# Kernel tuning notes

Measured on AMD Instinct MI355X. Metric: run time of the kernel, lower is better.

## Reference

```python
import jax, jax.numpy as jnp
import numpy as np

N = 100000
E = 1600000
D = 64  # in = hidden = out channels


def setup_inputs() -> dict:
    key = jax.random.key(0)
    ks = jax.random.split(key, 6)
    x = jax.random.normal(ks[0], (N, D), dtype=jnp.float32)
    edge_index = jax.random.randint(ks[1], (2, E), 0, N, dtype=jnp.int64)
    # bias-free linear weights, torch Linear layout [out, in]
    s = 1.0 / np.sqrt(D)
    W0 = jax.random.uniform(ks[2], (D, D), jnp.float32, -s, s)
    W1 = jax.random.uniform(ks[3], (D, D), jnp.float32, -s, s)
    Wm = jax.random.uniform(ks[4], (D, D), jnp.float32, -s, s)
    eps0 = jnp.zeros((), jnp.float32)  # train_eps=True, init 0.0
    eps1 = jnp.zeros((), jnp.float32)
    return {"x": x, "edge_index": edge_index, "W0": W0, "eps0": eps0,
            "W1": W1, "eps1": eps1, "Wm": Wm}


def reference(x, edge_index, W0, eps0, W1, eps1, Wm):
    n = x.shape[0]
    src, dst = edge_index[0], edge_index[1]

    def gin_conv(h, W, eps):
        # sparse adjacency sum-aggregation: out[i] = sum_{j->i} h[j]
        agg = jax.ops.segment_sum(h[src], dst, num_segments=n)
        # eps-scaled self-loop + bias-free linear
        return (agg + (1.0 + eps) * h) @ W.T

    h1 = jax.nn.relu(gin_conv(x, W0, eps0))   # xs[0], [N, D]
    h2 = jax.nn.relu(gin_conv(h1, W1, eps1))  # xs[1], [N, D]
    return (h1 @ Wm.T + h2) / 2.0
```

## Files before the change

kernel.cpp:

```cpp
#include <hip/hip_runtime.h>


__global__ __launch_bounds__(256) void zero_int_kernel(int* __restrict__ p, int n)
{
    int i = blockIdx.x * blockDim.x + threadIdx.x;
    int stride = gridDim.x * blockDim.x;
    for (; i < n; i += stride) p[i] = 0;
}

__global__ __launch_bounds__(256) void hist_rank_kernel(
    const int* __restrict__ dst, int* __restrict__ deg,
    int* __restrict__ rank, int E)
{
    int base = (blockIdx.x * blockDim.x + threadIdx.x) * 8;
    if (base + 7 < E) {
        int4 a = *(const int4*)&dst[base];
        int4 b = *(const int4*)&dst[base + 4];
        int r0 = atomicAdd(&deg[a.x], 1);
        int r1 = atomicAdd(&deg[a.y], 1);
        int r2 = atomicAdd(&deg[a.z], 1);
        int r3 = atomicAdd(&deg[a.w], 1);
        int r4 = atomicAdd(&deg[b.x], 1);
        int r5 = atomicAdd(&deg[b.y], 1);
        int r6 = atomicAdd(&deg[b.z], 1);
        int r7 = atomicAdd(&deg[b.w], 1);
        *(int4*)&rank[base]     = make_int4(r0, r1, r2, r3);
        *(int4*)&rank[base + 4] = make_int4(r4, r5, r6, r7);
    } else {
        for (int e = base; e < E; ++e) rank[e] = atomicAdd(&deg[dst[e]], 1);
    }
}

__global__ __launch_bounds__(256) void hist_kernel(
    const int* __restrict__ dst, int* __restrict__ deg, int E)
{
    int e4 = (blockIdx.x * blockDim.x + threadIdx.x) * 4;
    if (e4 + 3 < E) {
        int4 d = *(const int4*)&dst[e4];
        atomicAdd(&deg[d.x], 1);
        atomicAdd(&deg[d.y], 1);
        atomicAdd(&deg[d.z], 1);
        atomicAdd(&deg[d.w], 1);
    } else {
        for (int e = e4; e < E; ++e) atomicAdd(&deg[dst[e]], 1);
    }
}

__global__ __launch_bounds__(256) void scanA_kernel(
    const int* __restrict__ deg, int* __restrict__ off,
    int* __restrict__ bsum, int n)
{
    __shared__ int tmp[256];
    int t = threadIdx.x;
    int base = blockIdx.x * 1024 + t * 4;
    int v0 = 0, v1 = 0, v2 = 0, v3 = 0;
    if (base + 3 < n) {
        int4 q = *(const int4*)&deg[base];
        v0 = q.x; v1 = q.y; v2 = q.z; v3 = q.w;
    } else {
        if (base + 0 < n) v0 = deg[base + 0];
        if (base + 1 < n) v1 = deg[base + 1];
        if (base + 2 < n) v2 = deg[base + 2];
    }
    int tot = v0 + v1 + v2 + v3;
    tmp[t] = tot;
    __syncthreads();
    for (int d = 1; d < 256; d <<= 1) {
        int x = (t >= d) ? tmp[t - d] : 0;
        __syncthreads();
        tmp[t] += x;
        __syncthreads();
    }
    int incl = tmp[t];
    int p = incl - tot;
    if (base + 0 < n) off[base + 0] = p;
    if (base + 1 < n) off[base + 1] = p + v0;
    if (base + 2 < n) off[base + 2] = p + v0 + v1;
    if (base + 3 < n) off[base + 3] = p + v0 + v1 + v2;
    if (t == 255) bsum[blockIdx.x] = incl;
}

__global__ __launch_bounds__(256) void scanB_kernel(int* __restrict__ bsum, int nb)
{
    __shared__ int tmp[256];
    int t = threadIdx.x;
    int v = (t < nb) ? bsum[t] : 0;
    tmp[t] = v;
    __syncthreads();
    for (int d = 1; d < 256; d <<= 1) {
        int x = (t >= d) ? tmp[t - d] : 0;
        __syncthreads();
        tmp[t] += x;
        __syncthreads();
    }
    if (t < nb) bsum[t] = tmp[t] - v;
}

__global__ __launch_bounds__(256) void scanC_kernel(
    int* __restrict__ off, int* __restrict__ cursor,
    const int* __restrict__ bsum, int n, int E)
{
    int t = threadIdx.x;
    int add = bsum[blockIdx.x];
    int base = blockIdx.x * 1024 + t * 4;
#pragma unroll
    for (int q = 0; q < 4; ++q) {
        int idx = base + q;
        if (idx < n) {
            int v = off[idx] + add;
            off[idx] = v;
            if (cursor) cursor[idx] = v;
        }
    }
    if (blockIdx.x == 0 && t == 0) off[n] = E;
}

__global__ __launch_bounds__(256) void fill_rank_kernel(
    const int* __restrict__ src, const int* __restrict__ dst,
    const int* __restrict__ rank, const int* __restrict__ off,
    int* __restrict__ bucket, int E)
{
    int base = (blockIdx.x * blockDim.x + threadIdx.x) * 4;
    if (base + 3 < E) {
        int4 d = *(const int4*)&dst[base];
        int4 r = *(const int4*)&rank[base];
        int4 s = *(const int4*)&src[base];
        bucket[off[d.x] + r.x] = s.x;
        bucket[off[d.y] + r.y] = s.y;
        bucket[off[d.z] + r.z] = s.z;
        bucket[off[d.w] + r.w] = s.w;
    } else {
        for (int e = base; e < E; ++e) bucket[off[dst[e]] + rank[e]] = src[e];
    }
}

__global__ __launch_bounds__(256) void fill_kernel(
    const int* __restrict__ src, const int* __restrict__ dst,
    int* __restrict__ cursor, int* __restrict__ bucket, int E)
{
    int e = blockIdx.x * blockDim.x + threadIdx.x;
    if (e < E) {
        int d = dst[e];
        int p = atomicAdd(&cursor[d], 1);
        bucket[p] = src[e];
    }
}

#define WPB 8

__global__ __launch_bounds__(512) void fused_gin_kernel(
    const float* __restrict__ h, const int* __restrict__ off,
    const int* __restrict__ bucket, const float* __restrict__ W,
    const float* __restrict__ eps, float* __restrict__ out, int n)
{
    __shared__ float Ws[64][68];
    __shared__ float P[WPB][4][64];
    __shared__ float rowbuf[WPB][64];
    int tid = threadIdx.x;
    for (int idx = tid; idx < 4096; idx += 512) Ws[idx >> 6][idx & 63] = W[idx];
    __syncthreads();
    float s = 1.0f + eps[0];
    int lane = tid & 63;
    int w = tid >> 6;
    int l16 = lane & 15;
    int g = lane >> 4;
    int wavesTotal = gridDim.x * WPB;
    for (int i = blockIdx.x * WPB + w; i < n; i += wavesTotal) {
        float4 self4 = *(const float4*)&h[(size_t)i * 64 + l16 * 4];
        float4 acc4;
        if (g == 0) acc4 = make_float4(s * self4.x, s * self4.y, s * self4.z, s * self4.w);
        else        acc4 = make_float4(0.f, 0.f, 0.f, 0.f);

        int2 be = *(const int2*)&off[i];
        int beg = __builtin_amdgcn_readfirstlane(be.x);
        int end = __builtin_amdgcn_readfirstlane(be.y);
        int j = beg;
        for (; j + 8 <= end; j += 8) {
            int sa = bucket[j + g];
            int sb = bucket[j + 4 + g];
            float4 va = *(const float4*)&h[(size_t)sa * 64 + l16 * 4];
            float4 vb = *(const float4*)&h[(size_t)sb * 64 + l16 * 4];
            acc4.x += va.x + vb.x;
            acc4.y += va.y + vb.y;
            acc4.z += va.z + vb.z;
            acc4.w += va.w + vb.w;
        }
        if (j + 4 <= end) {
            int sa = bucket[j + g];
            float4 va = *(const float4*)&h[(size_t)sa * 64 + l16 * 4];
            acc4.x += va.x; acc4.y += va.y; acc4.z += va.z; acc4.w += va.w;
            j += 4;
        }
        if (j < end) {
            int jj = j + g;
            int sc = bucket[(jj < end) ? jj : (end - 1)];
            float m = (jj < end) ? 1.0f : 0.0f;
            float4 vc = *(const float4*)&h[(size_t)sc * 64 + l16 * 4];
            acc4.x = fmaf(vc.x, m, acc4.x);
            acc4.y = fmaf(vc.y, m, acc4.y);
            acc4.z = fmaf(vc.z, m, acc4.z);
            acc4.w = fmaf(vc.w, m, acc4.w);
        }
        *(float4*)&P[w][g][l16 * 4] = acc4;
        __builtin_amdgcn_wave_barrier();
        float r0 = P[w][0][lane], r1 = P[w][1][lane];
        float r2 = P[w][2][lane], r3 = P[w][3][lane];
        rowbuf[w][lane] = (r0 + r1) + (r2 + r3);
        __builtin_amdgcn_wave_barrier();
        const float4* wrow = (const float4*)&Ws[lane][0];
        const float4* rrow = (const float4*)&rowbuf[w][0];
        float o = 0.f;
#pragma unroll
        for (int k4 = 0; k4 < 16; ++k4) {
            float4 ww = wrow[k4];
            float4 rr = rrow[k4];
            o += ww.x * rr.x + ww.y * rr.y + ww.z * rr.z + ww.w * rr.w;
        }
        out[(size_t)i * 64 + lane] = fmaxf(o, 0.f);
        __builtin_amdgcn_wave_barrier();
    }
}

__global__ __launch_bounds__(512) void fused_final_csr_kernel(
    const float* __restrict__ h1, const int* __restrict__ off,
    const int* __restrict__ bucket, const float* __restrict__ W1,
    const float* __restrict__ Wm, const float* __restrict__ eps,
    float* __restrict__ out, int n)
{
    __shared__ float W1s[64][68];
    __shared__ float Wms[64][68];
    __shared__ float P[WPB][4][64];
    __shared__ float rowbuf[WPB][64];
    __shared__ float selfbuf[WPB][64];
    int tid = threadIdx.x;
    for (int idx = tid; idx < 4096; idx += 512) {
        W1s[idx >> 6][idx & 63] = W1[idx];
        Wms[idx >> 6][idx & 63] = Wm[idx];
    }
    __syncthreads();
    float s = 1.0f + eps[0];
    int lane = tid & 63;
    int w = tid >> 6;
    int l16 = lane & 15;
    int g = lane >> 4;
    int wavesTotal = gridDim.x * WPB;
    for (int i = blockIdx.x * WPB + w; i < n; i += wavesTotal) {
        float4 self4 = *(const float4*)&h1[(size_t)i * 64 + l16 * 4];
        float4 acc4;
        if (g == 0) acc4 = make_float4(s * self4.x, s * self4.y, s * self4.z, s * self4.w);
        else        acc4 = make_float4(0.f, 0.f, 0.f, 0.f);
        if (g == 0) *(float4*)&selfbuf[w][l16 * 4] = self4;

        int2 be = *(const int2*)&off[i];
        int beg = __builtin_amdgcn_readfirstlane(be.x);
        int end = __builtin_amdgcn_readfirstlane(be.y);
        int j = beg;
        for (; j + 8 <= end; j += 8) {
            int sa = bucket[j + g];
            int sb = bucket[j + 4 + g];
            float4 va = *(const float4*)&h1[(size_t)sa * 64 + l16 * 4];
            float4 vb = *(const float4*)&h1[(size_t)sb * 64 + l16 * 4];
            acc4.x += va.x + vb.x;
            acc4.y += va.y + vb.y;
            acc4.z += va.z + vb.z;
            acc4.w += va.w + vb.w;
        }
        if (j + 4 <= end) {
            int sa = bucket[j + g];
            float4 va = *(const float4*)&h1[(size_t)sa * 64 + l16 * 4];
            acc4.x += va.x; acc4.y += va.y; acc4.z += va.z; acc4.w += va.w;
            j += 4;
        }
        if (j < end) {
            int jj = j + g;
            int sc = bucket[(jj < end) ? jj : (end - 1)];
            float m = (jj < end) ? 1.0f : 0.0f;
            float4 vc = *(const float4*)&h1[(size_t)sc * 64 + l16 * 4];
            acc4.x = fmaf(vc.x, m, acc4.x);
            acc4.y = fmaf(vc.y, m, acc4.y);
            acc4.z = fmaf(vc.z, m, acc4.z);
            acc4.w = fmaf(vc.w, m, acc4.w);
        }
        *(float4*)&P[w][g][l16 * 4] = acc4;
        __builtin_amdgcn_wave_barrier();
        float r0 = P[w][0][lane], r1 = P[w][1][lane];
        float r2 = P[w][2][lane], r3 = P[w][3][lane];
        rowbuf[w][lane] = (r0 + r1) + (r2 + r3);
        __builtin_amdgcn_wave_barrier();
        const float4* w1row = (const float4*)&W1s[lane][0];
        const float4* wmrow = (const float4*)&Wms[lane][0];
        const float4* rrow  = (const float4*)&rowbuf[w][0];
        const float4* srow  = (const float4*)&selfbuf[w][0];
        float o1 = 0.f, o2 = 0.f;
#pragma unroll
        for (int k4 = 0; k4 < 16; ++k4) {
            float4 w1 = w1row[k4];
            float4 wm = wmrow[k4];
            float4 rr = rrow[k4];
            float4 sv = srow[k4];
            o1 += w1.x * rr.x + w1.y * rr.y + w1.z * rr.z + w1.w * rr.w;
            o2 += wm.x * sv.x + wm.y * sv.y + wm.z * sv.z + wm.w * sv.w;
        }
        out[(size_t)i * 64 + lane] = (fmaxf(o1, 0.f) + o2) * 0.5f;
        __builtin_amdgcn_wave_barrier();
    }
}

__global__ __launch_bounds__(256) void init_scale_kernel(
    const float* __restrict__ h, const float* __restrict__ eps,
    float* __restrict__ agg, int total4)
{
    float s = 1.0f + eps[0];
    int i = blockIdx.x * blockDim.x + threadIdx.x;
    int stride = gridDim.x * blockDim.x;
    const float4* h4 = (const float4*)h;
    float4* a4 = (float4*)agg;
    for (; i < total4; i += stride) {
        float4 v = h4[i];
        v.x *= s; v.y *= s; v.z *= s; v.w *= s;
        a4[i] = v;
    }
}

__global__ __launch_bounds__(256) void scatter_kernel(
    const float* __restrict__ h, const int* __restrict__ src,
    const int* __restrict__ dst, float* __restrict__ agg, int E)
{
    int lane = threadIdx.x & 63;
    int e = blockIdx.x * 4 + (threadIdx.x >> 6);
    if (e >= E) return;
    int s = src[e];
    int d = dst[e];
    atomicAdd(&agg[(size_t)d * 64 + lane], h[(size_t)s * 64 + lane]);
}

__global__ __launch_bounds__(256) void gemm_relu_kernel(
    const float* __restrict__ A, const float* __restrict__ W,
    float* __restrict__ out, int n)
{
    __shared__ float Wt[64][65];
    __shared__ float rowbuf[4][64];
    int tid = threadIdx.x;
    for (int i = tid; i < 4096; i += 256) Wt[i & 63][i >> 6] = W[i];
    __syncthreads();
    int lane = tid & 63;
    int w = tid >> 6;
    int wavesTotal = gridDim.x * 4;
    for (int i = blockIdx.x * 4 + w; i < n; i += wavesTotal) {
        rowbuf[w][lane] = A[(size_t)i * 64 + lane];
        __builtin_amdgcn_wave_barrier();
        float o = 0.f;
#pragma unroll
        for (int k = 0; k < 64; ++k) o += rowbuf[w][k] * Wt[k][lane];
        out[(size_t)i * 64 + lane] = fmaxf(o, 0.f);
        __builtin_amdgcn_wave_barrier();
    }
}

__global__ __launch_bounds__(256) void final_kernel(
    const float* __restrict__ Agg, const float* __restrict__ H1,
    const float* __restrict__ W1, const float* __restrict__ Wm,
    float* __restrict__ out, int n)
{
    __shared__ float W1t[64][65];
    __shared__ float Wmt[64][65];
    __shared__ float rowbuf[4][64];
    __shared__ float selfbuf[4][64];
    int tid = threadIdx.x;
    for (int i = tid; i < 4096; i += 256) {
        W1t[i & 63][i >> 6] = W1[i];
        Wmt[i & 63][i >> 6] = Wm[i];
    }
    __syncthreads();
    int lane = tid & 63;
    int w = tid >> 6;
    int wavesTotal = gridDim.x * 4;
    for (int i = blockIdx.x * 4 + w; i < n; i += wavesTotal) {
        rowbuf[w][lane] = Agg[(size_t)i * 64 + lane];
        selfbuf[w][lane] = H1[(size_t)i * 64 + lane];
        __builtin_amdgcn_wave_barrier();
        float o1 = 0.f, o2 = 0.f;
#pragma unroll
        for (int k = 0; k < 64; ++k) {
            o1 += rowbuf[w][k] * W1t[k][lane];
            o2 += selfbuf[w][k] * Wmt[k][lane];
        }
        out[(size_t)i * 64 + lane] = (fmaxf(o1, 0.f) + o2) * 0.5f;
        __builtin_amdgcn_wave_barrier();
    }
}

extern "C" void kernel_launch(void* const* d_in, const int* in_sizes, int n_in,
                              void* d_out, int out_size, void* d_ws, size_t ws_size,
                              hipStream_t stream)
{
    const float* x    = (const float*)d_in[0];
    const int*   ei   = (const int*)d_in[1];
    const float* W0   = (const float*)d_in[2];
    const float* eps0 = (const float*)d_in[3];
    const float* W1   = (const float*)d_in[4];
    const float* eps1 = (const float*)d_in[5];
    const float* Wm   = (const float*)d_in[6];
    float* out = (float*)d_out;

    int n = in_sizes[0] / 64;
    int E = in_sizes[1] / 2;
    const int* src = ei;
    const int* dst = ei + E;

    auto align1k = [](size_t v) { return (v + 1023) & ~(size_t)1023; };
    size_t h1_off     = 0;
    size_t off_off    = align1k(h1_off + (size_t)n * 64 * 4);
    size_t deg_off    = align1k(off_off + (size_t)(n + 1) * 4);
    size_t cursor_off = align1k(deg_off + (size_t)n * 4);
    size_t bsum_off   = align1k(cursor_off + (size_t)n * 4);
    size_t bucket_off = align1k(bsum_off + 256 * 4);
    size_t rank_off   = align1k(bucket_off + (size_t)E * 4);
    size_t need_B     = rank_off;
    size_t need_A     = rank_off + (size_t)E * 4;

    int nb = (n + 1023) / 1024;
    int e4Blocks = (E + 1023) / 1024;
    int e8Blocks = (E + 2047) / 2048;

    if (ws_size >= need_B) {
        float* h1    = (float*)((char*)d_ws + h1_off);
        int* off     = (int*)((char*)d_ws + off_off);
        int* deg     = (int*)((char*)d_ws + deg_off);
        int* cursor  = (int*)((char*)d_ws + cursor_off);
        int* bsum    = (int*)((char*)d_ws + bsum_off);
        int* bucket  = (int*)((char*)d_ws + bucket_off);
        int* rank    = (int*)((char*)d_ws + rank_off);

        zero_int_kernel<<<256, 256, 0, stream>>>(deg, n);
        if (ws_size >= need_A) {
            hist_rank_kernel<<<e8Blocks, 256, 0, stream>>>(dst, deg, rank, E);
            scanA_kernel<<<nb, 256, 0, stream>>>(deg, off, bsum, n);
            scanB_kernel<<<1, 256, 0, stream>>>(bsum, nb);
            scanC_kernel<<<nb, 256, 0, stream>>>(off, (int*)nullptr, bsum, n, E);
            fill_rank_kernel<<<e4Blocks, 256, 0, stream>>>(src, dst, rank, off, bucket, E);
        } else {
            hist_kernel<<<e4Blocks, 256, 0, stream>>>(dst, deg, E);
            scanA_kernel<<<nb, 256, 0, stream>>>(deg, off, bsum, n);
            scanB_kernel<<<1, 256, 0, stream>>>(bsum, nb);
            scanC_kernel<<<nb, 256, 0, stream>>>(off, cursor, bsum, n, E);
            fill_kernel<<<(E + 255) / 256, 256, 0, stream>>>(src, dst, cursor, bucket, E);
        }

        fused_gin_kernel<<<1024, 512, 0, stream>>>(x, off, bucket, W0, eps0, h1, n);
        fused_final_csr_kernel<<<768, 512, 0, stream>>>(h1, off, bucket, W1, Wm, eps1, out, n);
    } else {
        float* agg = (float*)d_ws;
        float* h1  = out;
        int total4 = n * 16;
        int scatterBlocks = (E + 3) / 4;

        init_scale_kernel<<<2048, 256, 0, stream>>>(x, eps0, agg, total4);
        scatter_kernel<<<scatterBlocks, 256, 0, stream>>>(x, src, dst, agg, E);
        gemm_relu_kernel<<<2048, 256, 0, stream>>>(agg, W0, h1, n);
        init_scale_kernel<<<2048, 256, 0, stream>>>(h1, eps1, agg, total4);
        scatter_kernel<<<scatterBlocks, 256, 0, stream>>>(h1, src, dst, agg, E);
        final_kernel<<<2048, 256, 0, stream>>>(agg, h1, W1, Wm, out, n);
    }
}
```

Before: 251.2 us.

## Batch four rows per wave in GIN kernels and widen CSR build per-thread work

Each wave in both fused GIN kernels now gathers four destination rows before running the 64x64 matvec. Weight rows read from shared memory are reused across the four rows, and the cross-group reduction of partial sums uses xor shuffles in place of a shared-memory staging buffer. The histogram-rank kernel now handles 16 edges per thread and the fill kernel 8, with grid sizes adjusted to match. In exchange the kernels use more registers, which may lower occupancy and reduce load-balancing granularity.

```diff
diff --git a/kernel.cpp b/kernel.cpp
--- a/kernel.cpp
+++ b/kernel.cpp
@@ -12,10 +12,12 @@
     const int* __restrict__ dst, int* __restrict__ deg,
     int* __restrict__ rank, int E)
 {
-    int base = (blockIdx.x * blockDim.x + threadIdx.x) * 8;
-    if (base + 7 < E) {
+    int base = (blockIdx.x * blockDim.x + threadIdx.x) * 16;
+    if (base + 15 < E) {
         int4 a = *(const int4*)&dst[base];
         int4 b = *(const int4*)&dst[base + 4];
+        int4 c = *(const int4*)&dst[base + 8];
+        int4 d = *(const int4*)&dst[base + 12];
         int r0 = atomicAdd(&deg[a.x], 1);
         int r1 = atomicAdd(&deg[a.y], 1);
         int r2 = atomicAdd(&deg[a.z], 1);
@@ -24,8 +26,18 @@
         int r5 = atomicAdd(&deg[b.y], 1);
         int r6 = atomicAdd(&deg[b.z], 1);
         int r7 = atomicAdd(&deg[b.w], 1);
-        *(int4*)&rank[base]     = make_int4(r0, r1, r2, r3);
-        *(int4*)&rank[base + 4] = make_int4(r4, r5, r6, r7);
+        int r8 = atomicAdd(&deg[c.x], 1);
+        int r9 = atomicAdd(&deg[c.y], 1);
+        int rA = atomicAdd(&deg[c.z], 1);
+        int rB = atomicAdd(&deg[c.w], 1);
+        int rC = atomicAdd(&deg[d.x], 1);
+        int rD = atomicAdd(&deg[d.y], 1);
+        int rE = atomicAdd(&deg[d.z], 1);
+        int rF = atomicAdd(&deg[d.w], 1);
+        *(int4*)&rank[base]      = make_int4(r0, r1, r2, r3);
+        *(int4*)&rank[base + 4]  = make_int4(r4, r5, r6, r7);
+        *(int4*)&rank[base + 8]  = make_int4(r8, r9, rA, rB);
+        *(int4*)&rank[base + 12] = make_int4(rC, rD, rE, rF);
     } else {
         for (int e = base; e < E; ++e) rank[e] = atomicAdd(&deg[dst[e]], 1);
     }
@@ -120,15 +132,22 @@
     const int* __restrict__ rank, const int* __restrict__ off,
     int* __restrict__ bucket, int E)
 {
-    int base = (blockIdx.x * blockDim.x + threadIdx.x) * 4;
-    if (base + 3 < E) {
-        int4 d = *(const int4*)&dst[base];
-        int4 r = *(const int4*)&rank[base];
-        int4 s = *(const int4*)&src[base];
-        bucket[off[d.x] + r.x] = s.x;
-        bucket[off[d.y] + r.y] = s.y;
-        bucket[off[d.z] + r.z] = s.z;
-        bucket[off[d.w] + r.w] = s.w;
+    int base = (blockIdx.x * blockDim.x + threadIdx.x) * 8;
+    if (base + 7 < E) {
+        int4 d0 = *(const int4*)&dst[base];
+        int4 d1 = *(const int4*)&dst[base + 4];
+        int4 r0 = *(const int4*)&rank[base];
+        int4 r1 = *(const int4*)&rank[base + 4];
+        int4 s0 = *(const int4*)&src[base];
+        int4 s1 = *(const int4*)&src[base + 4];
+        bucket[off[d0.x] + r0.x] = s0.x;
+        bucket[off[d0.y] + r0.y] = s0.y;
+        bucket[off[d0.z] + r0.z] = s0.z;
+        bucket[off[d0.w] + r0.w] = s0.w;
+        bucket[off[d1.x] + r1.x] = s1.x;
+        bucket[off[d1.y] + r1.y] = s1.y;
+        bucket[off[d1.z] + r1.z] = s1.z;
+        bucket[off[d1.w] + r1.w] = s1.w;
     } else {
         for (int e = base; e < E; ++e) bucket[off[dst[e]] + rank[e]] = src[e];
     }
@@ -147,6 +166,55 @@
 }
 
 #define WPB 8
+#define NT  4
+
+__device__ __forceinline__ float dot4(float4 a, float4 b)
+{
+    return a.x * b.x + a.y * b.y + a.z * b.z + a.w * b.w;
+}
+
+__device__ __forceinline__ float4 gather_row(
+    const float* __restrict__ h, const int* __restrict__ bucket,
+    int beg, int end, int g, int l16, float4 init)
+{
+    float4 acc4 = init;
+    int j = beg;
+    for (; j + 8 <= end; j += 8) {
+        int sa = bucket[j + g];
+        int sb = bucket[j + 4 + g];
+        float4 va = *(const float4*)&h[(size_t)sa * 64 + l16 * 4];
+        float4 vb = *(const float4*)&h[(size_t)sb * 64 + l16 * 4];
+        acc4.x += va.x + vb.x;
+        acc4.y += va.y + vb.y;
+        acc4.z += va.z + vb.z;
+        acc4.w += va.w + vb.w;
+    }
+    if (j + 4 <= end) {
+        int sa = bucket[j + g];
+        float4 va = *(const float4*)&h[(size_t)sa * 64 + l16 * 4];
+        acc4.x += va.x; acc4.y += va.y; acc4.z += va.z; acc4.w += va.w;
+        j += 4;
+    }
+    if (j < end) {
+        int jj = j + g;
+        int sc = bucket[(jj < end) ? jj : (end - 1)];
+        float m = (jj < end) ? 1.0f : 0.0f;
+        float4 vc = *(const float4*)&h[(size_t)sc * 64 + l16 * 4];
+        acc4.x = fmaf(vc.x, m, acc4.x);
+        acc4.y = fmaf(vc.y, m, acc4.y);
+        acc4.z = fmaf(vc.z, m, acc4.z);
+        acc4.w = fmaf(vc.w, m, acc4.w);
+    }
+    acc4.x += __shfl_xor(acc4.x, 16, 64);
+    acc4.y += __shfl_xor(acc4.y, 16, 64);
+    acc4.z += __shfl_xor(acc4.z, 16, 64);
+    acc4.w += __shfl_xor(acc4.w, 16, 64);
+    acc4.x += __shfl_xor(acc4.x, 32, 64);
+    acc4.y += __shfl_xor(acc4.y, 32, 64);
+    acc4.z += __shfl_xor(acc4.z, 32, 64);
+    acc4.w += __shfl_xor(acc4.w, 32, 64);
+    return acc4;
+}
 
 __global__ __launch_bounds__(512) void fused_gin_kernel(
     const float* __restrict__ h, const int* __restrict__ off,
@@ -154,8 +222,7 @@
     const float* __restrict__ eps, float* __restrict__ out, int n)
 {
     __shared__ float Ws[64][68];
-    __shared__ float P[WPB][4][64];
-    __shared__ float rowbuf[WPB][64];
+    __shared__ float rowbuf[WPB][NT][64];
     int tid = threadIdx.x;
     for (int idx = tid; idx < 4096; idx += 512) Ws[idx >> 6][idx & 63] = W[idx];
     __syncthreads();
@@ -164,59 +231,40 @@
     int w = tid >> 6;
     int l16 = lane & 15;
     int g = lane >> 4;
-    int wavesTotal = gridDim.x * WPB;
-    for (int i = blockIdx.x * WPB + w; i < n; i += wavesTotal) {
-        float4 self4 = *(const float4*)&h[(size_t)i * 64 + l16 * 4];
-        float4 acc4;
-        if (g == 0) acc4 = make_float4(s * self4.x, s * self4.y, s * self4.z, s * self4.w);
-        else        acc4 = make_float4(0.f, 0.f, 0.f, 0.f);
-
-        int2 be = *(const int2*)&off[i];
-        int beg = __builtin_amdgcn_readfirstlane(be.x);
-        int end = __builtin_amdgcn_readfirstlane(be.y);
-        int j = beg;
-        for (; j + 8 <= end; j += 8) {
-            int sa = bucket[j + g];
-            int sb = bucket[j + 4 + g];
-            float4 va = *(const float4*)&h[(size_t)sa * 64 + l16 * 4];
-            float4 vb = *(const float4*)&h[(size_t)sb * 64 + l16 * 4];
-            acc4.x += va.x + vb.x;
-            acc4.y += va.y + vb.y;
-            acc4.z += va.z + vb.z;
-            acc4.w += va.w + vb.w;
-        }
-        if (j + 4 <= end) {
-            int sa = bucket[j + g];
-            float4 va = *(const float4*)&h[(size_t)sa * 64 + l16 * 4];
-            acc4.x += va.x; acc4.y += va.y; acc4.z += va.z; acc4.w += va.w;
-            j += 4;
-        }
-        if (j < end) {
-            int jj = j + g;
-            int sc = bucket[(jj < end) ? jj : (end - 1)];
-            float m = (jj < end) ? 1.0f : 0.0f;
-            float4 vc = *(const float4*)&h[(size_t)sc * 64 + l16 * 4];
-            acc4.x = fmaf(vc.x, m, acc4.x);
-            acc4.y = fmaf(vc.y, m, acc4.y);
-            acc4.z = fmaf(vc.z, m, acc4.z);
-            acc4.w = fmaf(vc.w, m, acc4.w);
-        }
-        *(float4*)&P[w][g][l16 * 4] = acc4;
-        __builtin_amdgcn_wave_barrier();
-        float r0 = P[w][0][lane], r1 = P[w][1][lane];
-        float r2 = P[w][2][lane], r3 = P[w][3][lane];
-        rowbuf[w][lane] = (r0 + r1) + (r2 + r3);
+    int stride = gridDim.x * WPB * NT;
+    for (int i0 = (blockIdx.x * WPB + w) * NT; i0 < n; i0 += stride) {
+#pragma unroll
+        for (int t = 0; t < NT; ++t) {
+            int i = i0 + t;
+            if (i >= n) break;
+            float4 init = make_float4(0.f, 0.f, 0.f, 0.f);
+            if (g == 0) {
+                float4 self4 = *(const float4*)&h[(size_t)i * 64 + l16 * 4];
+                init = make_float4(s * self4.x, s * self4.y, s * self4.z, s * self4.w);
+            }
+            int2 be = *(const int2*)&off[i];
+            int beg = __builtin_amdgcn_readfirstlane(be.x);
+            int end = __builtin_amdgcn_readfirstlane(be.y);
+            float4 red = gather_row(h, bucket, beg, end, g, l16, init);
+            if (g == 0) *(float4*)&rowbuf[w][t][l16 * 4] = red;
+        }
         __builtin_amdgcn_wave_barrier();
         const float4* wrow = (const float4*)&Ws[lane][0];
-        const float4* rrow = (const float4*)&rowbuf[w][0];
-        float o = 0.f;
+        float o[NT] = {0.f, 0.f, 0.f, 0.f};
 #pragma unroll
         for (int k4 = 0; k4 < 16; ++k4) {
             float4 ww = wrow[k4];
-            float4 rr = rrow[k4];
-            o += ww.x * rr.x + ww.y * rr.y + ww.z * rr.z + ww.w * rr.w;
-        }
-        out[(size_t)i * 64 + lane] = fmaxf(o, 0.f);
+#pragma unroll
+            for (int t = 0; t < NT; ++t) {
+                float4 rr = *(const float4*)&rowbuf[w][t][k4 * 4];
+                o[t] += dot4(ww, rr);
+            }
+        }
+#pragma unroll
+        for (int t = 0; t < NT; ++t) {
+            int i = i0 + t;
+            if (i < n) out[(size_t)i * 64 + lane] = fmaxf(o[t], 0.f);
+        }
         __builtin_amdgcn_wave_barrier();
     }
 }
@@ -229,9 +277,8 @@
 {
     __shared__ float W1s[64][68];
     __shared__ float Wms[64][68];
-    __shared__ float P[WPB][4][64];
-    __shared__ float rowbuf[WPB][64];
-    __shared__ float selfbuf[WPB][64];
+    __shared__ float rowbuf[WPB][NT][64];
+    __shared__ float selfbuf[WPB][NT][64];
     int tid = threadIdx.x;
     for (int idx = tid; idx < 4096; idx += 512) {
         W1s[idx >> 6][idx & 63] = W1[idx];
@@ -243,65 +290,46 @@
     int w = tid >> 6;
     int l16 = lane & 15;
     int g = lane >> 4;
-    int wavesTotal = gridDim.x * WPB;
-    for (int i = blockIdx.x * WPB + w; i < n; i += wavesTotal) {
-        float4 self4 = *(const float4*)&h1[(size_t)i * 64 + l16 * 4];
-        float4 acc4;
-        if (g == 0) acc4 = make_float4(s * self4.x, s * self4.y, s * self4.z, s * self4.w);
-        else        acc4 = make_float4(0.f, 0.f, 0.f, 0.f);
-        if (g == 0) *(float4*)&selfbuf[w][l16 * 4] = self4;
-
-        int2 be = *(const int2*)&off[i];
-        int beg = __builtin_amdgcn_readfirstlane(be.x);
-        int end = __builtin_amdgcn_readfirstlane(be.y);
-        int j = beg;
-        for (; j + 8 <= end; j += 8) {
-            int sa = bucket[j + g];
-            int sb = bucket[j + 4 + g];
-            float4 va = *(const float4*)&h1[(size_t)sa * 64 + l16 * 4];
-            float4 vb = *(const float4*)&h1[(size_t)sb * 64 + l16 * 4];
-            acc4.x += va.x + vb.x;
-            acc4.y += va.y + vb.y;
-            acc4.z += va.z + vb.z;
-            acc4.w += va.w + vb.w;
-        }
-        if (j + 4 <= end) {
-            int sa = bucket[j + g];
-            float4 va = *(const float4*)&h1[(size_t)sa * 64 + l16 * 4];
-            acc4.x += va.x; acc4.y += va.y; acc4.z += va.z; acc4.w += va.w;
-            j += 4;
-        }
-        if (j < end) {
-            int jj = j + g;
-            int sc = bucket[(jj < end) ? jj : (end - 1)];
-            float m = (jj < end) ? 1.0f : 0.0f;
-            float4 vc = *(const float4*)&h1[(size_t)sc * 64 + l16 * 4];
-            acc4.x = fmaf(vc.x, m, acc4.x);
-            acc4.y = fmaf(vc.y, m, acc4.y);
-            acc4.z = fmaf(vc.z, m, acc4.z);
-            acc4.w = fmaf(vc.w, m, acc4.w);
-        }
-        *(float4*)&P[w][g][l16 * 4] = acc4;
-        __builtin_amdgcn_wave_barrier();
-        float r0 = P[w][0][lane], r1 = P[w][1][lane];
-        float r2 = P[w][2][lane], r3 = P[w][3][lane];
-        rowbuf[w][lane] = (r0 + r1) + (r2 + r3);
+    int stride = gridDim.x * WPB * NT;
+    for (int i0 = (blockIdx.x * WPB + w) * NT; i0 < n; i0 += stride) {
+#pragma unroll
+        for (int t = 0; t < NT; ++t) {
+            int i = i0 + t;
+            if (i >= n) break;
+            float4 init = make_float4(0.f, 0.f, 0.f, 0.f);
+            if (g == 0) {
+                float4 self4 = *(const float4*)&h1[(size_t)i * 64 + l16 * 4];
+                *(float4*)&selfbuf[w][t][l16 * 4] = self4;
+                init = make_float4(s * self4.x, s * self4.y, s * self4.z, s * self4.w);
+            }
+            int2 be = *(const int2*)&off[i];
+            int beg = __builtin_amdgcn_readfirstlane(be.x);
+            int end = __builtin_amdgcn_readfirstlane(be.y);
+            float4 red = gather_row(h1, bucket, beg, end, g, l16, init);
+            if (g == 0) *(float4*)&rowbuf[w][t][l16 * 4] = red;
+        }
         __builtin_amdgcn_wave_barrier();
         const float4* w1row = (const float4*)&W1s[lane][0];
         const float4* wmrow = (const float4*)&Wms[lane][0];
-        const float4* rrow  = (const float4*)&rowbuf[w][0];
-        const float4* srow  = (const float4*)&selfbuf[w][0];
-        float o1 = 0.f, o2 = 0.f;
+        float o1[NT] = {0.f, 0.f, 0.f, 0.f};
+        float o2[NT] = {0.f, 0.f, 0.f, 0.f};
 #pragma unroll
         for (int k4 = 0; k4 < 16; ++k4) {
-            float4 w1 = w1row[k4];
-            float4 wm = wmrow[k4];
-            float4 rr = rrow[k4];
-            float4 sv = srow[k4];
-            o1 += w1.x * rr.x + w1.y * rr.y + w1.z * rr.z + w1.w * rr.w;
-            o2 += wm.x * sv.x + wm.y * sv.y + wm.z * sv.z + wm.w * sv.w;
-        }
-        out[(size_t)i * 64 + lane] = (fmaxf(o1, 0.f) + o2) * 0.5f;
+            float4 w1v = w1row[k4];
+            float4 wmv = wmrow[k4];
+#pragma unroll
+            for (int t = 0; t < NT; ++t) {
+                float4 rr = *(const float4*)&rowbuf[w][t][k4 * 4];
+                float4 sv = *(const float4*)&selfbuf[w][t][k4 * 4];
+                o1[t] += dot4(w1v, rr);
+                o2[t] += dot4(wmv, sv);
+            }
+        }
+#pragma unroll
+        for (int t = 0; t < NT; ++t) {
+            int i = i0 + t;
+            if (i < n) out[(size_t)i * 64 + lane] = (fmaxf(o1[t], 0.f) + o2[t]) * 0.5f;
+        }
         __builtin_amdgcn_wave_barrier();
     }
 }
@@ -420,8 +448,9 @@
     size_t need_A     = rank_off + (size_t)E * 4;
 
     int nb = (n + 1023) / 1024;
-    int e4Blocks = (E + 1023) / 1024;
-    int e8Blocks = (E + 2047) / 2048;
+    int e4Blocks  = (E + 1023) / 1024;
+    int e8Blocks  = (E + 2047) / 2048;
+    int e16Blocks = (E + 4095) / 4096;
 
     if (ws_size >= need_B) {
         float* h1    = (float*)((char*)d_ws + h1_off);
@@ -434,11 +463,11 @@
 
         zero_int_kernel<<<256, 256, 0, stream>>>(deg, n);
         if (ws_size >= need_A) {
-            hist_rank_kernel<<<e8Blocks, 256, 0, stream>>>(dst, deg, rank, E);
+            hist_rank_kernel<<<e16Blocks, 256, 0, stream>>>(dst, deg, rank, E);
             scanA_kernel<<<nb, 256, 0, stream>>>(deg, off, bsum, n);
             scanB_kernel<<<1, 256, 0, stream>>>(bsum, nb);
             scanC_kernel<<<nb, 256, 0, stream>>>(off, (int*)nullptr, bsum, n, E);
-            fill_rank_kernel<<<e4Blocks, 256, 0, stream>>>(src, dst, rank, off, bucket, E);
+            fill_rank_kernel<<<e8Blocks, 256, 0, stream>>>(src, dst, rank, off, bucket, E);
         } else {
             hist_kernel<<<e4Blocks, 256, 0, stream>>>(dst, deg, E);
             scanA_kernel<<<nb, 256, 0, stream>>>(deg, off, bsum, n);
```

New measurement: 949.3 us. 3.78x slower.
